# Optimization experiments

Hardware: AMD Instinct MI355X
Metric: run time of the kernel (lower is better)

## Reference

```python
import jax, jax.numpy as jnp
import numpy as np
import math

B, T, C, H = 2, 2048, 512, 8
K, DIL = 3, 1
EPS = 1e-5


def _ln(x, g, b):
    m = jnp.mean(x, axis=-1, keepdims=True)
    v = jnp.mean(jnp.square(x - m), axis=-1, keepdims=True)
    return (x - m) * jax.lax.rsqrt(v + EPS) * g + b


def setup_inputs() -> dict:
    key = jax.random.key(0)
    ks = jax.random.split(key, 12)
    s = 0.02
    return {
        "x": jax.random.normal(ks[0], (B, T, C), jnp.float32),
        "conv_w": jax.random.normal(ks[1], (C, C, K), jnp.float32) * s,  # OIH
        "conv_b": jax.random.normal(ks[2], (C,), jnp.float32) * s,
        "g1": jnp.ones((C,), jnp.float32), "b1": jnp.zeros((C,), jnp.float32),
        "qkv_w": jax.random.normal(ks[3], (C, 3 * C), jnp.float32) * s,
        "qkv_b": jax.random.normal(ks[4], (3 * C,), jnp.float32) * s,
        "proj_w": jax.random.normal(ks[5], (C, C), jnp.float32) * s,
        "proj_b": jax.random.normal(ks[6], (C,), jnp.float32) * s,
        "g2": jnp.ones((C,), jnp.float32), "b2": jnp.zeros((C,), jnp.float32),
        "ffn_w1": jax.random.normal(ks[7], (C, 2 * C), jnp.float32) * s,
        "ffn_b1": jax.random.normal(ks[8], (2 * C,), jnp.float32) * s,
        "ffn_w2": jax.random.normal(ks[9], (2 * C, C), jnp.float32) * s,
        "ffn_b2": jax.random.normal(ks[10], (C,), jnp.float32) * s,
        "g3": jnp.ones((C,), jnp.float32), "b3": jnp.zeros((C,), jnp.float32),
    }


def reference(x, conv_w, conv_b, g1, b1, qkv_w, qkv_b, proj_w, proj_b,
              g2, b2, ffn_w1, ffn_b1, ffn_w2, ffn_b2, g3, b3):
    b, t, c = x.shape
    hd = c // H
    # --- causal dilated conv (left-pad only == pad both + right-trim) ---
    pad = (K - 1) * DIL
    xc = jnp.transpose(x, (0, 2, 1))  # [B,C,T]
    conv = jax.lax.conv_general_dilated(
        xc, conv_w, window_strides=(1,), padding=[(pad, 0)],
        rhs_dilation=(DIL,), dimension_numbers=("NCH", "OIH", "NCH"))
    conv = conv + conv_b[None, :, None]
    x = _ln(x + jnp.transpose(conv, (0, 2, 1)), g1, b1)
    # --- causal self-attention ---
    qkv = (x @ qkv_w + qkv_b).reshape(b, t, 3, H, hd)
    qkv = jnp.transpose(qkv, (2, 0, 3, 1, 4))  # [3,B,H,T,hd]
    q, k, v = qkv[0], qkv[1], qkv[2]
    scores = jnp.einsum("bhqd,bhkd->bhqk", q, k) / math.sqrt(hd)
    causal = jnp.tril(jnp.ones((t, t), bool))
    scores = jnp.where(causal, scores, -jnp.inf)
    attn = jax.nn.softmax(scores, axis=-1)
    out = jnp.einsum("bhqk,bhkd->bhqd", attn, v)
    out = jnp.transpose(out, (0, 2, 1, 3)).reshape(b, t, c)
    out = out @ proj_w + proj_b
    x = _ln(x + out, g2, b2)
    # --- FFN ---
    ffn = jax.nn.relu(x @ ffn_w1 + ffn_b1) @ ffn_w2 + ffn_b2
    return _ln(x + ffn, g3, b3)
```

## Files before the change

kernel.cpp:

```cpp
#include <hip/hip_runtime.h>
#include <hip/hip_bf16.h>

#define TT 2048
#define QSC 0.18033688011112042f

typedef __attribute__((ext_vector_type(4))) float f32x4;
typedef __attribute__((ext_vector_type(8))) __bf16 bf16x8;
typedef __attribute__((ext_vector_type(4))) short short4v;
typedef __attribute__((ext_vector_type(8))) short short8v;

enum { M_CONV = 0, M_QKV = 1, M_PROJ = 2, M_FFN1 = 3, M_FFN2 = 4 };

__device__ __forceinline__ void gload16(const void* g, void* l) {
    __builtin_amdgcn_global_load_lds(
        (__attribute__((address_space(1))) void*)g,
        (__attribute__((address_space(3))) void*)l, 16, 0, 0);
}

__device__ __forceinline__ short f2bf(float f) {
    unsigned u = __float_as_uint(f);
    u = (u + 0x7fffu + ((u >> 16) & 1u)) >> 16;
    return (short)u;
}

__device__ __forceinline__ float bf2f(short s) {
    unsigned u = ((unsigned)(unsigned short)s) << 16;
    return __uint_as_float(u);
}

__global__ __launch_bounds__(256) void prep_all(
    const float* __restrict__ conv_w, const float* __restrict__ x,
    const float* __restrict__ qkv_w, const float* __restrict__ proj_w,
    const float* __restrict__ f1w, const float* __restrict__ f2w,
    short* __restrict__ cwT, short* __restrict__ xpad,
    short* __restrict__ qkvT, short* __restrict__ projT,
    short* __restrict__ f1T, short* __restrict__ f2T) {
    if (blockIdx.x < 2048) {
        int t = blockIdx.x;
        const float* src; short* dst; int K, N, lt;
        if (t < 768)       { src = qkv_w;  dst = qkvT;  K = 512;  N = 1536; lt = t; }
        else if (t < 1024) { src = proj_w; dst = projT; K = 512;  N = 512;  lt = t - 768; }
        else if (t < 1536) { src = f1w;    dst = f1T;   K = 512;  N = 1024; lt = t - 1024; }
        else               { src = f2w;    dst = f2T;   K = 1024; N = 512;  lt = t - 1536; }
        int ntn = N >> 5;
        int kt = lt / ntn, nt = lt - kt * ntn;
        int k0 = kt * 32, n0 = nt * 32;
        __shared__ float tile[32][33];
        int c = threadIdx.x & 31, r = threadIdx.x >> 5;
        #pragma unroll
        for (int i = 0; i < 4; i++)
            tile[r + i * 8][c] = src[(size_t)(k0 + r + i * 8) * N + n0 + c];
        __syncthreads();
        #pragma unroll
        for (int i = 0; i < 4; i++)
            dst[(size_t)(n0 + r + i * 8) * K + k0 + c] = f2bf(tile[c][r + i * 8]);
        return;
    }
    if (blockIdx.x < 3072) {
        int oi = (blockIdx.x - 2048) * 256 + threadIdx.x;
        int o = oi >> 9, i = oi & 511;
        const float* s = conv_w + (size_t)oi * 3;
        #pragma unroll
        for (int tap = 0; tap < 3; tap++)
            cwT[(size_t)o * 1536 + tap * 512 + i] = f2bf(s[tap]);
        return;
    }
    int idx = (blockIdx.x - 3072) * 256 + threadIdx.x;
    int rp = idx >> 6, j = idx & 63;
    if (rp < 4100) {
        int bb = rp / 2050, rr = rp - bb * 2050;
        int t = rr - 2;
        short8v pk;
        if (t >= 0) {
            const float* xs = x + ((size_t)(bb << 11) + t) * 512 + j * 8;
            f32x4 a = *(const f32x4*)xs;
            f32x4 b2 = *(const f32x4*)(xs + 4);
            #pragma unroll
            for (int i = 0; i < 4; i++) { pk[i] = f2bf(a[i]); pk[i + 4] = f2bf(b2[i]); }
        } else {
            #pragma unroll
            for (int i = 0; i < 8; i++) pk[i] = 0;
        }
        *(short8v*)&xpad[(size_t)rp * 512 + j * 8] = pk;
    }
}

__global__ __launch_bounds__(512) void ln_row(const short* __restrict__ in,
                                              const float* __restrict__ g,
                                              const float* __restrict__ b,
                                              float* __restrict__ outf,
                                              short* __restrict__ outb) {
    int row = blockIdx.x * 8 + (threadIdx.x >> 6);
    int l = threadIdx.x & 63;
    short8v v = *(const short8v*)(in + (size_t)row * 512 + l * 8);
    float vf[8];
    float s = 0.f, ss = 0.f;
    #pragma unroll
    for (int i = 0; i < 8; i++) {
        vf[i] = bf2f(v[i]);
        s += vf[i]; ss += vf[i] * vf[i];
    }
    #pragma unroll
    for (int off = 1; off < 64; off <<= 1) {
        s  += __shfl_xor(s, off);
        ss += __shfl_xor(ss, off);
    }
    float mean = s * (1.f / 512);
    float var  = ss * (1.f / 512) - mean * mean;
    float rstd = rsqrtf(var + 1e-5f);
    f32x4 g0 = *(const f32x4*)(g + l * 8), g1 = *(const f32x4*)(g + l * 8 + 4);
    f32x4 b0 = *(const f32x4*)(b + l * 8), b1 = *(const f32x4*)(b + l * 8 + 4);
    float ov[8];
    #pragma unroll
    for (int i = 0; i < 4; i++) {
        ov[i]     = (vf[i]     - mean) * rstd * g0[i] + b0[i];
        ov[i + 4] = (vf[i + 4] - mean) * rstd * g1[i] + b1[i];
    }
    if (outf) {
        float* q = outf + (size_t)row * 512 + l * 8;
        *(f32x4*)q       = (f32x4){ov[0], ov[1], ov[2], ov[3]};
        *(f32x4*)(q + 4) = (f32x4){ov[4], ov[5], ov[6], ov[7]};
    }
    if (outb) {
        short8v pk;
        #pragma unroll
        for (int i = 0; i < 8; i++) pk[i] = f2bf(ov[i]);
        *(short8v*)(outb + (size_t)row * 512 + l * 8) = pk;
    }
}

template<int MODE>
__device__ __forceinline__ const short* a_ptr(const short* A, int m0, int r, int kk, int K) {
    if constexpr (MODE == M_CONV) {
        int row = m0 + r;
        int bb = row >> 11, t5 = row & 2047;
        int tap = kk >> 9, k2 = kk & 511;
        return A + ((size_t)(bb * 2050 + t5 + tap) * 512 + k2);
    } else {
        return A + ((size_t)(m0 + r) * K + kk);
    }
}

template<int MODE, int BM, int BN, int BK>
__global__ __launch_bounds__((BM == 64) ? 128 : 256) void gemm_mfma(
    const short* __restrict__ A, const short* __restrict__ Bw,
    const float* __restrict__ bias, const void* __restrict__ res,
    void* __restrict__ Cout, short* __restrict__ vTb, int K) {
    constexpr int NT  = (BM == 64) ? 128 : 256;
    constexpr int MF  = (BM == 64) ? 2 : 4;
    constexpr int NF  = 2;
    constexpr int KCH = BK / 32;
    constexpr int CPR = BK / 8;
    constexpr int CSH = (BK == 64) ? 3 : 4;
    constexpr int CMSK = CPR - 1;
    constexpr int ACH = (BM * BK * 2) / (16 * NT);
    constexpr int BCH = (BN * BK * 2) / (16 * NT);
    __shared__ short As[BM * BK];
    __shared__ short Bs[BN * BK];
    const int tid = threadIdx.x;
    const int w = tid >> 6, l = tid & 63;
    const int lr = l & 15, lc = l >> 4;
    const int wrb = (BM == 64) ? (w * 32) : ((w >> 1) * 64);
    const int wcb = (BM == 64) ? 0 : ((w & 1) * 32);
    const int m0 = blockIdx.x * BM, n0 = blockIdx.y * BN;
    f32x4 acc[MF][NF];
    #pragma unroll
    for (int mf = 0; mf < MF; mf++)
        #pragma unroll
        for (int nf = 0; nf < NF; nf++) acc[mf][nf] = (f32x4){0.f, 0.f, 0.f, 0.f};

    for (int k0 = 0; k0 < K; k0 += BK) {
        #pragma unroll
        for (int i = 0; i < ACH; i++) {
            int u = i * NT + tid, r = u >> CSH, c = (u & CMSK) ^ (r & 7);
            gload16(a_ptr<MODE>(A, m0, r, k0 + c * 8, K), (char*)As + u * 16);
        }
        #pragma unroll
        for (int i = 0; i < BCH; i++) {
            int u = i * NT + tid, r = u >> CSH, c = (u & CMSK) ^ (r & 7);
            gload16(Bw + ((size_t)(n0 + r) * K + k0 + c * 8), (char*)Bs + u * 16);
        }
        __syncthreads();
        bf16x8 af[MF][KCH], bfv[NF][KCH];
        #pragma unroll
        for (int mf = 0; mf < MF; mf++)
            #pragma unroll
            for (int ks = 0; ks < KCH; ks++) {
                int rr = wrb + mf * 16 + lr;
                int cc = (ks * 4 + lc) ^ (rr & 7);
                af[mf][ks] = *(const bf16x8*)&As[rr * BK + cc * 8];
            }
        #pragma unroll
        for (int nf = 0; nf < NF; nf++)
            #pragma unroll
            for (int ks = 0; ks < KCH; ks++) {
                int rr = wcb + nf * 16 + lr;
                int cc = (ks * 4 + lc) ^ (rr & 7);
                bfv[nf][ks] = *(const bf16x8*)&Bs[rr * BK + cc * 8];
            }
        __builtin_amdgcn_s_setprio(1);
        #pragma unroll
        for (int nf = 0; nf < NF; nf++)
            #pragma unroll
            for (int ks = 0; ks < KCH; ks++)
                #pragma unroll
                for (int mf = 0; mf < MF; mf++)
                    acc[mf][nf] = __builtin_amdgcn_mfma_f32_16x16x32_bf16(
                        af[mf][ks], bfv[nf][ks], acc[mf][nf], 0, 0, 0);
        __builtin_amdgcn_s_setprio(0);
        __syncthreads();
    }
    #pragma unroll
    for (int mf = 0; mf < MF; mf++) {
        int row0 = m0 + wrb + mf * 16 + lc * 4;
        #pragma unroll
        for (int nf = 0; nf < NF; nf++) {
            int col = n0 + wcb + nf * 16 + lr;
            float bv = bias[col];
            if constexpr (MODE == M_CONV) {
                short* Cb = (short*)Cout;
                const float* rf = (const float*)res;
                #pragma unroll
                for (int rg = 0; rg < 4; rg++) {
                    size_t off = (size_t)(row0 + rg) * 512 + col;
                    Cb[off] = f2bf(acc[mf][nf][rg] + bv + rf[off]);
                }
            } else if constexpr (MODE == M_PROJ || MODE == M_FFN2) {
                short* Cb = (short*)Cout;
                const short* rb = (const short*)res;
                #pragma unroll
                for (int rg = 0; rg < 4; rg++) {
                    size_t off = (size_t)(row0 + rg) * 512 + col;
                    Cb[off] = f2bf(acc[mf][nf][rg] + bv + bf2f(rb[off]));
                }
            } else if constexpr (MODE == M_FFN1) {
                short* Cb = (short*)Cout;
                #pragma unroll
                for (int rg = 0; rg < 4; rg++)
                    Cb[(size_t)(row0 + rg) * 1024 + col] =
                        f2bf(fmaxf(acc[mf][nf][rg] + bv, 0.f));
            } else {
                short* Cb = (short*)Cout;
                float v[4];
                #pragma unroll
                for (int rg = 0; rg < 4; rg++) {
                    v[rg] = acc[mf][nf][rg] + bv;
                    float wv = (col < 512) ? v[rg] * QSC : v[rg];
                    Cb[(size_t)(row0 + rg) * 1536 + col] = f2bf(wv);
                }
                if (col >= 1024) {
                    int vc = col - 1024, hh = vc >> 6, dd = vc & 63;
                    int bb = row0 >> 11, t5 = row0 & 2047;
                    short4v pk = {f2bf(v[0]), f2bf(v[1]), f2bf(v[2]), f2bf(v[3])};
                    *(short4v*)&vTb[((size_t)((bb << 3) + hh) * 64 + dd) * 2048 + t5] = pk;
                }
            }
        }
    }
}

__global__ __launch_bounds__(256) void attn_part(const short* __restrict__ qkvb,
                                                 const short* __restrict__ vTb,
                                                 short* __restrict__ pO,
                                                 float* __restrict__ pML) {
    __shared__ short SM[20992];
    __bf16* SMb = (__bf16*)SM;
    const int tid = threadIdx.x;
    const int w = tid >> 6, l = tid & 63;
    const int lr = l & 15, lc = l >> 4;
    const int L = blockIdx.x;
    const int bh = L & 15;
    const int par = (L >> 4) & 3;
    const int qt = 31 - (L >> 6);
    const int b = bh >> 3, h = bh & 7;
    const int qr = w * 16, q0 = qt * 64;
    const int pbase = 16384 + w * (16 * 72);
    const int ntiles = (qt >= par) ? ((qt - par) >> 2) + 1 : 0;

    #pragma unroll
    for (int i = 0; i < 2; i++) {
        int u = i * 256 + tid, r = u >> 3, c = (u & 7) ^ (r & 7);
        gload16(qkvb + ((size_t)(b * 2048 + q0 + r) * 1536 + h * 64 + c * 8),
                (char*)&SM[16384] + u * 16);
        if (ntiles > 0) {
            gload16(qkvb + ((size_t)(b * 2048 + par * 64 + r) * 1536 + 512 + h * 64 + c * 8),
                    (char*)&SM[0] + u * 16);
            gload16(vTb + ((size_t)(bh * 64 + r) * 2048 + par * 64 + c * 8),
                    (char*)&SM[8192] + u * 16);
        }
    }
    __syncthreads();
    bf16x8 aq[2];
    #pragma unroll
    for (int ks = 0; ks < 2; ks++) {
        int rr = qr + lr;
        int cc = (lc + 4 * ks) ^ (rr & 7);
        aq[ks] = *(const bf16x8*)&SM[16384 + rr * 64 + cc * 8];
    }
    __syncthreads();

    bf16x8 onesf;
    #pragma unroll
    for (int i = 0; i < 8; i++) onesf[i] = (__bf16)1.0f;

    f32x4 o[4], lacc;
    float mst[4];
    #pragma unroll
    for (int nf = 0; nf < 4; nf++) o[nf] = (f32x4){0.f, 0.f, 0.f, 0.f};
    lacc = (f32x4){0.f, 0.f, 0.f, 0.f};
    #pragma unroll
    for (int rg = 0; rg < 4; rg++) mst[rg] = -1e30f;

    for (int s = 0; s < ntiles; s++) {
        const int kt = par + 4 * s;
        const int cur = s & 1;
        if (s + 1 < ntiles) {
            int ktn = kt + 4, nb = (cur ^ 1) * 4096;
            #pragma unroll
            for (int i = 0; i < 2; i++) {
                int u = i * 256 + tid, r = u >> 3, c = (u & 7) ^ (r & 7);
                gload16(qkvb + ((size_t)(b * 2048 + ktn * 64 + r) * 1536 + 512 + h * 64 + c * 8),
                        (char*)&SM[nb] + u * 16);
                gload16(vTb + ((size_t)(bh * 64 + r) * 2048 + ktn * 64 + c * 8),
                        (char*)&SM[8192 + nb] + u * 16);
            }
        }
        f32x4 s4[4];
        #pragma unroll
        for (int nf = 0; nf < 4; nf++) s4[nf] = (f32x4){0.f, 0.f, 0.f, 0.f};
        __builtin_amdgcn_s_setprio(1);
        #pragma unroll
        for (int nf = 0; nf < 4; nf++) {
            #pragma unroll
            for (int ks = 0; ks < 2; ks++) {
                int rr = nf * 16 + lr;
                int cc = (lc + 4 * ks) ^ (rr & 7);
                bf16x8 bk = *(const bf16x8*)&SM[cur * 4096 + rr * 64 + cc * 8];
                s4[nf] = __builtin_amdgcn_mfma_f32_16x16x32_bf16(aq[ks], bk, s4[nf], 0, 0, 0);
            }
        }
        __builtin_amdgcn_s_setprio(0);
        const bool diag = (kt == qt);
        if (diag) {
            #pragma unroll
            for (int nf = 0; nf < 4; nf++)
                #pragma unroll
                for (int rg = 0; rg < 4; rg++)
                    if (nf * 16 + lr > qr + lc * 4 + rg) s4[nf][rg] = -1e30f;
        }
        float rm[4];
        int ok = 1;
        #pragma unroll
        for (int rg = 0; rg < 4; rg++) {
            float m_ = fmaxf(fmaxf(s4[0][rg], s4[1][rg]), fmaxf(s4[2][rg], s4[3][rg]));
            m_ = fmaxf(m_, __shfl_xor(m_, 1));
            m_ = fmaxf(m_, __shfl_xor(m_, 2));
            m_ = fmaxf(m_, __shfl_xor(m_, 4));
            m_ = fmaxf(m_, __shfl_xor(m_, 8));
            rm[rg] = m_;
            ok &= (m_ <= mst[rg] + 11.5f);
        }
        if (!__all(ok)) {
            #pragma unroll
            for (int rg = 0; rg < 4; rg++) {
                float mn = fmaxf(mst[rg], rm[rg]);
                float alpha = exp2f(mst[rg] - mn);
                mst[rg] = mn;
                lacc[rg] *= alpha;
                #pragma unroll
                for (int nf = 0; nf < 4; nf++) o[nf][rg] *= alpha;
            }
        }
        #pragma unroll
        for (int rg = 0; rg < 4; rg++) {
            int prow = pbase + (lc * 4 + rg) * 72;
            SMb[prow      + lr] = (__bf16)exp2f(s4[0][rg] - mst[rg]);
            SMb[prow + 16 + lr] = (__bf16)exp2f(s4[1][rg] - mst[rg]);
            SMb[prow + 32 + lr] = (__bf16)exp2f(s4[2][rg] - mst[rg]);
            SMb[prow + 48 + lr] = (__bf16)exp2f(s4[3][rg] - mst[rg]);
        }
        bf16x8 pa[2];
        #pragma unroll
        for (int ks = 0; ks < 2; ks++)
            pa[ks] = *(const bf16x8*)&SM[pbase + lr * 72 + ks * 32 + lc * 8];
        __builtin_amdgcn_s_setprio(1);
        #pragma unroll
        for (int ks = 0; ks < 2; ks++)
            lacc = __builtin_amdgcn_mfma_f32_16x16x32_bf16(pa[ks], onesf, lacc, 0, 0, 0);
        #pragma unroll
        for (int nf = 0; nf < 4; nf++) {
            #pragma unroll
            for (int ks = 0; ks < 2; ks++) {
                int rr = nf * 16 + lr;
                int cc = (lc + 4 * ks) ^ (rr & 7);
                bf16x8 bv = *(const bf16x8*)&SM[8192 + cur * 4096 + rr * 64 + cc * 8];
                o[nf] = __builtin_amdgcn_mfma_f32_16x16x32_bf16(pa[ks], bv, o[nf], 0, 0, 0);
            }
        }
        __builtin_amdgcn_s_setprio(0);
        __syncthreads();
    }

    size_t ob = (size_t)L * 4096;
    #pragma unroll
    for (int nf = 0; nf < 4; nf++) {
        #pragma unroll
        for (int rg = 0; rg < 4; rg++) {
            int rw = qr + lc * 4 + rg;
            pO[ob + rw * 64 + nf * 16 + lr] = (ntiles > 0) ? f2bf(o[nf][rg]) : (short)0;
        }
    }
    if (lr == 0) {
        #pragma unroll
        for (int rg = 0; rg < 4; rg++) {
            int rw = qr + lc * 4 + rg;
            pML[(size_t)L * 128 + rw]      = (ntiles > 0) ? mst[rg] : -1e30f;
            pML[(size_t)L * 128 + 64 + rw] = (ntiles > 0) ? lacc[rg] : 0.f;
        }
    }
}

__global__ __launch_bounds__(256) void attn_merge(const short* __restrict__ pO,
                                                  const float* __restrict__ pML,
                                                  short* __restrict__ aout) {
    int U = blockIdx.x;
    int bh = U & 15, qt = U >> 4;
    int b = bh >> 3, h = bh & 7, q0 = qt * 64;
    int Lb = ((31 - qt) << 6) | bh;
    int t = threadIdx.x;
    int r = t >> 2, cs = (t & 3) * 16;
    float m[4], lv[4];
    #pragma unroll
    for (int pp = 0; pp < 4; pp++) {
        m[pp]  = pML[(size_t)(Lb | (pp << 4)) * 128 + r];
        lv[pp] = pML[(size_t)(Lb | (pp << 4)) * 128 + 64 + r];
    }
    float mn = fmaxf(fmaxf(m[0], m[1]), fmaxf(m[2], m[3]));
    float a[4], den = 0.f;
    #pragma unroll
    for (int pp = 0; pp < 4; pp++) { a[pp] = exp2f(m[pp] - mn); den += lv[pp] * a[pp]; }
    float inv = 1.f / den;
    #pragma unroll
    for (int half = 0; half < 2; half++) {
        int c0 = cs + half * 8;
        float accv[8];
        #pragma unroll
        for (int j = 0; j < 8; j++) accv[j] = 0.f;
        #pragma unroll
        for (int pp = 0; pp < 4; pp++) {
            short8v ov = *(const short8v*)&pO[(size_t)(Lb | (pp << 4)) * 4096 + r * 64 + c0];
            #pragma unroll
            for (int j = 0; j < 8; j++) accv[j] += bf2f(ov[j]) * a[pp];
        }
        short8v res;
        #pragma unroll
        for (int j = 0; j < 8; j++) res[j] = f2bf(accv[j] * inv);
        *(short8v*)&aout[(size_t)(b * 2048 + q0 + r) * 512 + h * 64 + c0] = res;
    }
}

extern "C" void kernel_launch(void* const* d_in, const int* in_sizes, int n_in,
                              void* d_out, int out_size, void* d_ws, size_t ws_size,
                              hipStream_t stream) {
    const float* x      = (const float*)d_in[0];
    const float* conv_w = (const float*)d_in[1];
    const float* conv_b = (const float*)d_in[2];
    const float* g1     = (const float*)d_in[3];
    const float* b1     = (const float*)d_in[4];
    const float* qkv_w  = (const float*)d_in[5];
    const float* qkv_b  = (const float*)d_in[6];
    const float* proj_w = (const float*)d_in[7];
    const float* proj_b = (const float*)d_in[8];
    const float* g2     = (const float*)d_in[9];
    const float* b2     = (const float*)d_in[10];
    const float* ffn_w1 = (const float*)d_in[11];
    const float* ffn_b1 = (const float*)d_in[12];
    const float* ffn_w2 = (const float*)d_in[13];
    const float* ffn_b2 = (const float*)d_in[14];
    const float* g3     = (const float*)d_in[15];
    const float* b3     = (const float*)d_in[16];
    float* out = (float*)d_out;

    char* p = (char*)d_ws;
    short* cwT   = (short*)p;  p += 786432 * 2;
    short* qkvT  = (short*)p;  p += 786432 * 2;
    short* projT = (short*)p;  p += 262144 * 2;
    short* f1T   = (short*)p;  p += 524288 * 2;
    short* f2T   = (short*)p;  p += 524288 * 2;
    short* xpad  = (short*)p;  p += 2099200 * 2;
    short* yb    = (short*)p;  p += 2097152 * 2;
    short* x1b   = (short*)p;  p += 2097152 * 2;
    short* qkvb  = (short*)p;  p += 6291456 * 2;
    short* vTb   = (short*)p;  p += 2097152 * 2;
    short* pO    = (short*)p;  p += 8388608 * 2;
    float* pML   = (float*)p;  p += 262144 * 4;
    short* x2b     = x1b;
    short* hb      = qkvb;
    short* attnout = xpad;

    prep_all<<<4097, 256, 0, stream>>>(conv_w, x, qkv_w, proj_w, ffn_w1, ffn_w2,
                                       cwT, xpad, qkvT, projT, f1T, f2T);
    gemm_mfma<M_CONV, 64, 32, 128><<<dim3(64, 16), 128, 0, stream>>>(
        xpad, cwT, conv_b, x, yb, nullptr, 1536);
    ln_row<<<512, 512, 0, stream>>>(yb, g1, b1, nullptr, x1b);
    gemm_mfma<M_QKV, 128, 64, 64><<<dim3(32, 24), 256, 0, stream>>>(
        x1b, qkvT, qkv_b, nullptr, qkvb, vTb, 512);
    attn_part<<<2048, 256, 0, stream>>>(qkvb, vTb, pO, pML);
    attn_merge<<<512, 256, 0, stream>>>(pO, pML, attnout);
    gemm_mfma<M_PROJ, 64, 32, 128><<<dim3(64, 16), 128, 0, stream>>>(
        attnout, projT, proj_b, x1b, yb, nullptr, 512);
    ln_row<<<512, 512, 0, stream>>>(yb, g2, b2, nullptr, x2b);
    gemm_mfma<M_FFN1, 128, 64, 64><<<dim3(32, 16), 256, 0, stream>>>(
        x2b, f1T, ffn_b1, nullptr, hb, nullptr, 512);
    gemm_mfma<M_FFN2, 64, 32, 128><<<dim3(64, 16), 128, 0, stream>>>(
        hb, f2T, ffn_b2, x2b, yb, nullptr, 1024);
    ln_row<<<512, 512, 0, stream>>>(yb, g3, b3, out, nullptr);
}
```

Before: 118.1 us.

## Double-buffer LDS tiles in BM=64 GEMMs and halve their K tile

For the 64-row GEMM variants (conv, proj, FFN2), the k-loop now uses two LDS buffers. The next K tile is prefetched with global_load_lds while the current one feeds MFMA, using explicit vmcnt waits and raw s_barrier instead of __syncthreads. The K tile for these launches drops from 128 to 64, so the double buffer fits in a similar LDS footprint. The goal is to hide global load latency behind compute; the cost is more loop iterations and reliance on hand-counted vmcnt values, which must match the per-stage load count.

```diff
diff --git a/kernel.cpp b/kernel.cpp
--- a/kernel.cpp
+++ b/kernel.cpp
@@ -155,8 +155,9 @@
     constexpr int CMSK = CPR - 1;
     constexpr int ACH = (BM * BK * 2) / (16 * NT);
     constexpr int BCH = (BN * BK * 2) / (16 * NT);
-    __shared__ short As[BM * BK];
-    __shared__ short Bs[BN * BK];
+    constexpr int NBUF = (BM == 64) ? 2 : 1;
+    __shared__ short As[NBUF * BM * BK];
+    __shared__ short Bs[NBUF * BN * BK];
     const int tid = threadIdx.x;
     const int w = tid >> 6, l = tid & 63;
     const int lr = l & 15, lc = l >> 4;
@@ -169,46 +170,113 @@
         #pragma unroll
         for (int nf = 0; nf < NF; nf++) acc[mf][nf] = (f32x4){0.f, 0.f, 0.f, 0.f};
 
-    for (int k0 = 0; k0 < K; k0 += BK) {
+    const int nit = K / BK;
+    if constexpr (BM == 64) {
         #pragma unroll
         for (int i = 0; i < ACH; i++) {
             int u = i * NT + tid, r = u >> CSH, c = (u & CMSK) ^ (r & 7);
-            gload16(a_ptr<MODE>(A, m0, r, k0 + c * 8, K), (char*)As + u * 16);
+            gload16(a_ptr<MODE>(A, m0, r, c * 8, K), (char*)As + u * 16);
         }
         #pragma unroll
         for (int i = 0; i < BCH; i++) {
             int u = i * NT + tid, r = u >> CSH, c = (u & CMSK) ^ (r & 7);
-            gload16(Bw + ((size_t)(n0 + r) * K + k0 + c * 8), (char*)Bs + u * 16);
-        }
-        __syncthreads();
-        bf16x8 af[MF][KCH], bfv[NF][KCH];
-        #pragma unroll
-        for (int mf = 0; mf < MF; mf++)
-            #pragma unroll
-            for (int ks = 0; ks < KCH; ks++) {
-                int rr = wrb + mf * 16 + lr;
-                int cc = (ks * 4 + lc) ^ (rr & 7);
-                af[mf][ks] = *(const bf16x8*)&As[rr * BK + cc * 8];
-            }
-        #pragma unroll
-        for (int nf = 0; nf < NF; nf++)
-            #pragma unroll
-            for (int ks = 0; ks < KCH; ks++) {
-                int rr = wcb + nf * 16 + lr;
-                int cc = (ks * 4 + lc) ^ (rr & 7);
-                bfv[nf][ks] = *(const bf16x8*)&Bs[rr * BK + cc * 8];
-            }
-        __builtin_amdgcn_s_setprio(1);
-        #pragma unroll
-        for (int nf = 0; nf < NF; nf++)
-            #pragma unroll
-            for (int ks = 0; ks < KCH; ks++)
-                #pragma unroll
-                for (int mf = 0; mf < MF; mf++)
-                    acc[mf][nf] = __builtin_amdgcn_mfma_f32_16x16x32_bf16(
-                        af[mf][ks], bfv[nf][ks], acc[mf][nf], 0, 0, 0);
-        __builtin_amdgcn_s_setprio(0);
-        __syncthreads();
+            gload16(Bw + ((size_t)(n0 + r) * K + c * 8), (char*)Bs + u * 16);
+        }
+        for (int it = 0; it < nit; it++) {
+            const int cur = it & 1;
+            if (it + 1 < nit) {
+                int k0 = (it + 1) * BK;
+                int bo = (cur ^ 1);
+                #pragma unroll
+                for (int i = 0; i < ACH; i++) {
+                    int u = i * NT + tid, r = u >> CSH, c = (u & CMSK) ^ (r & 7);
+                    gload16(a_ptr<MODE>(A, m0, r, k0 + c * 8, K),
+                            (char*)As + bo * (BM * BK * 2) + u * 16);
+                }
+                #pragma unroll
+                for (int i = 0; i < BCH; i++) {
+                    int u = i * NT + tid, r = u >> CSH, c = (u & CMSK) ^ (r & 7);
+                    gload16(Bw + ((size_t)(n0 + r) * K + k0 + c * 8),
+                            (char*)Bs + bo * (BN * BK * 2) + u * 16);
+                }
+                asm volatile("s_waitcnt vmcnt(6)" ::: "memory");
+            } else {
+                asm volatile("s_waitcnt vmcnt(0)" ::: "memory");
+            }
+            __builtin_amdgcn_s_barrier();
+            __builtin_amdgcn_sched_barrier(0);
+            bf16x8 af[MF][KCH], bfv[NF][KCH];
+            #pragma unroll
+            for (int mf = 0; mf < MF; mf++)
+                #pragma unroll
+                for (int ks = 0; ks < KCH; ks++) {
+                    int rr = wrb + mf * 16 + lr;
+                    int cc = (ks * 4 + lc) ^ (rr & 7);
+                    af[mf][ks] = *(const bf16x8*)&As[cur * BM * BK + rr * BK + cc * 8];
+                }
+            #pragma unroll
+            for (int nf = 0; nf < NF; nf++)
+                #pragma unroll
+                for (int ks = 0; ks < KCH; ks++) {
+                    int rr = wcb + nf * 16 + lr;
+                    int cc = (ks * 4 + lc) ^ (rr & 7);
+                    bfv[nf][ks] = *(const bf16x8*)&Bs[cur * BN * BK + rr * BK + cc * 8];
+                }
+            __builtin_amdgcn_s_setprio(1);
+            #pragma unroll
+            for (int nf = 0; nf < NF; nf++)
+                #pragma unroll
+                for (int ks = 0; ks < KCH; ks++)
+                    #pragma unroll
+                    for (int mf = 0; mf < MF; mf++)
+                        acc[mf][nf] = __builtin_amdgcn_mfma_f32_16x16x32_bf16(
+                            af[mf][ks], bfv[nf][ks], acc[mf][nf], 0, 0, 0);
+            __builtin_amdgcn_s_setprio(0);
+            __builtin_amdgcn_s_barrier();
+        }
+    } else {
+        for (int it = 0; it < nit; it++) {
+            int k0 = it * BK;
+            #pragma unroll
+            for (int i = 0; i < ACH; i++) {
+                int u = i * NT + tid, r = u >> CSH, c = (u & CMSK) ^ (r & 7);
+                gload16(a_ptr<MODE>(A, m0, r, k0 + c * 8, K), (char*)As + u * 16);
+            }
+            #pragma unroll
+            for (int i = 0; i < BCH; i++) {
+                int u = i * NT + tid, r = u >> CSH, c = (u & CMSK) ^ (r & 7);
+                gload16(Bw + ((size_t)(n0 + r) * K + k0 + c * 8), (char*)Bs + u * 16);
+            }
+            __syncthreads();
+            bf16x8 af[MF][KCH], bfv[NF][KCH];
+            #pragma unroll
+            for (int mf = 0; mf < MF; mf++)
+                #pragma unroll
+                for (int ks = 0; ks < KCH; ks++) {
+                    int rr = wrb + mf * 16 + lr;
+                    int cc = (ks * 4 + lc) ^ (rr & 7);
+                    af[mf][ks] = *(const bf16x8*)&As[rr * BK + cc * 8];
+                }
+            #pragma unroll
+            for (int nf = 0; nf < NF; nf++)
+                #pragma unroll
+                for (int ks = 0; ks < KCH; ks++) {
+                    int rr = wcb + nf * 16 + lr;
+                    int cc = (ks * 4 + lc) ^ (rr & 7);
+                    bfv[nf][ks] = *(const bf16x8*)&Bs[rr * BK + cc * 8];
+                }
+            __builtin_amdgcn_s_setprio(1);
+            #pragma unroll
+            for (int nf = 0; nf < NF; nf++)
+                #pragma unroll
+                for (int ks = 0; ks < KCH; ks++)
+                    #pragma unroll
+                    for (int mf = 0; mf < MF; mf++)
+                        acc[mf][nf] = __builtin_amdgcn_mfma_f32_16x16x32_bf16(
+                            af[mf][ks], bfv[nf][ks], acc[mf][nf], 0, 0, 0);
+            __builtin_amdgcn_s_setprio(0);
+            __syncthreads();
+        }
     }
     #pragma unroll
     for (int mf = 0; mf < MF; mf++) {
@@ -500,19 +568,19 @@
 
     prep_all<<<4097, 256, 0, stream>>>(conv_w, x, qkv_w, proj_w, ffn_w1, ffn_w2,
                                        cwT, xpad, qkvT, projT, f1T, f2T);
-    gemm_mfma<M_CONV, 64, 32, 128><<<dim3(64, 16), 128, 0, stream>>>(
+    gemm_mfma<M_CONV, 64, 32, 64><<<dim3(64, 16), 128, 0, stream>>>(
         xpad, cwT, conv_b, x, yb, nullptr, 1536);
     ln_row<<<512, 512, 0, stream>>>(yb, g1, b1, nullptr, x1b);
     gemm_mfma<M_QKV, 128, 64, 64><<<dim3(32, 24), 256, 0, stream>>>(
         x1b, qkvT, qkv_b, nullptr, qkvb, vTb, 512);
     attn_part<<<2048, 256, 0, stream>>>(qkvb, vTb, pO, pML);
     attn_merge<<<512, 256, 0, stream>>>(pO, pML, attnout);
-    gemm_mfma<M_PROJ, 64, 32, 128><<<dim3(64, 16), 128, 0, stream>>>(
+    gemm_mfma<M_PROJ, 64, 32, 64><<<dim3(64, 16), 128, 0, stream>>>(
         attnout, projT, proj_b, x1b, yb, nullptr, 512);
     ln_row<<<512, 512, 0, stream>>>(yb, g2, b2, nullptr, x2b);
     gemm_mfma<M_FFN1, 128, 64, 64><<<dim3(32, 16), 256, 0, stream>>>(
         x2b, f1T, ffn_b1, nullptr, hb, nullptr, 512);
-    gemm_mfma<M_FFN2, 64, 32, 128><<<dim3(64, 16), 128, 0, stream>>>(
+    gemm_mfma<M_FFN2, 64, 32, 64><<<dim3(64, 16), 128, 0, stream>>>(
         hb, f2T, ffn_b2, x2b, yb, nullptr, 1024);
     ln_row<<<512, 512, 0, stream>>>(yb, g3, b3, out, nullptr);
 }
```

Measured after the change: 122.0 us. +3.3%, slower.
